# Kernel optimization log

Hardware: AMD Instinct MI355X
Metric: run time of the kernel (lower is better)

The kernel has to match this reference:

```python
import jax, jax.numpy as jnp
import numpy as np

B, L, DL, DM, K = 8192, 1, 1024, 1024, 8


def setup_inputs() -> dict:
    key = jax.random.key(0)
    ks = jax.random.split(key, 8)
    s = lambda k, shape, sc=1.0: jax.random.normal(k, shape, jnp.float32) * sc
    return {
        "l_hidden": s(ks[0], (B, L, DL)),
        "m_hidden": s(ks[1], (B, L, DM)),
        "G_l_m": s(ks[2], (DL, K, DM)),   # randn'd each fwd in torch; exposed as input
        "G_m_l": s(ks[3], (DM, K, DL)),
        "l_fc1_w": s(ks[4], (256, DL), 0.02),
        "l_fc1_b": jnp.zeros((256,), jnp.float32),
        "l_fc2_w": s(ks[5], (DL, 256), 0.02),
        "l_fc2_b": jnp.zeros((DL,), jnp.float32),
        "m_fc1_w": s(ks[6], (128, DM), 0.02),
        "m_fc1_b": jnp.zeros((128,), jnp.float32),
        "m_fc2_w": s(ks[7], (DM, 128), 0.02),
        "m_fc2_b": jnp.zeros((DM,), jnp.float32),
    }


def _cross(h_a, h_b, G, g_vec):
    """One direction of the cross-share unit.
    h_a: [B,L,Da], h_b: [B,L,Db], G: [Da,K,Db], g_vec: [B,L,Da]. L must be 1.
    Broadcasts G over batch instead of torch's .repeat (same math, no 256GB copy).
    """
    b, l, da = h_a.shape
    k = G.shape[1]
    # l_hidden @ reshape(G, [Da, K*Db]) -> reshape to [B, L*K, Db]
    s = jnp.einsum('bld,dke->blke', h_a, G).reshape(b, l * k, -1)      # [B,L*K,Db]
    # tanh( shared @ h_b^T ) -> [B, L*K, L]
    t = jnp.tanh(jnp.einsum('bke,bse->bks', s, h_b))                    # [B,L*K,L]
    # reshape [B,L,K,L] -> permute [B,L,L,K] -> [B,L*L,K]
    t = t.reshape(b, l, k, l).transpose(0, 1, 3, 2).reshape(b, l * l, k)
    g = jnp.tile(g_vec, (1, k, 1))                                      # [B,L*K,Da] (L=1 -> [B,K,Da])
    vec = jnp.matmul(t, g)                                              # [B,L*L,Da]
    attn = jax.nn.softmax(vec, axis=-1)
    out = h_a + attn * h_a
    return out, attn


def reference(l_hidden, m_hidden, G_l_m, G_m_l,
              l_fc1_w, l_fc1_b, l_fc2_w, l_fc2_b,
              m_fc1_w, m_fc1_b, m_fc2_w, m_fc2_b):
    # dropout(0.3) is identity in eval mode
    G_vec_l = (l_hidden @ l_fc1_w.T + l_fc1_b) @ l_fc2_w.T + l_fc2_b   # [B,L,DL]
    G_vec_m = (m_hidden @ m_fc1_w.T + m_fc1_b) @ m_fc2_w.T + m_fc2_b   # [B,L,DM]
    l_out, l_attn = _cross(l_hidden, m_hidden, G_l_m, G_vec_l)
    m_out, m_attn = _cross(m_hidden, l_hidden, G_m_l, G_vec_m)
    return l_out, m_out, l_attn, m_attn
```

## Files before the change

### kernel.cpp

```cpp
#include <hip/hip_runtime.h>


#define NB 8192
#define DD 1024

typedef __bf16 bf16x8 __attribute__((ext_vector_type(8)));
typedef float f32x4 __attribute__((ext_vector_type(4)));

__device__ __forceinline__ unsigned short f2bf(float f) {
  unsigned u = __float_as_uint(f);
  u += 0x7FFFu + ((u >> 16) & 1u);
  return (unsigned short)(u >> 16);
}
__device__ __forceinline__ float bf2f(unsigned short h) {
  return __uint_as_float(((unsigned)h) << 16);
}

__global__ __launch_bounds__(256) void split_cast_k(
    const float* __restrict__ in, unsigned short* __restrict__ hi,
    unsigned short* __restrict__ lo, int n4) {
  int i = blockIdx.x * 256 + threadIdx.x;
  if (i >= n4) return;
  float4 v = reinterpret_cast<const float4*>(in)[i];
  float vv[4] = {v.x, v.y, v.z, v.w};
  unsigned short hh[4], ll[4];
#pragma unroll
  for (int c = 0; c < 4; ++c) {
    hh[c] = f2bf(vv[c]);
    ll[c] = f2bf(vv[c] - bf2f(hh[c]));
  }
  reinterpret_cast<ushort4*>(hi)[i] = make_ushort4(hh[0], hh[1], hh[2], hh[3]);
  reinterpret_cast<ushort4*>(lo)[i] = make_ushort4(ll[0], ll[1], ll[2], ll[3]);
}

__global__ __launch_bounds__(256) void transpose_split_k(
    const float* __restrict__ G, unsigned short* __restrict__ bhi,
    unsigned short* __restrict__ blo) {
  __shared__ float t[32][33];
  int c0 = blockIdx.x * 32;
  int d0 = blockIdx.y * 32;
  int tx = threadIdx.x & 31;
  int tg = threadIdx.x >> 5;
#pragma unroll
  for (int s = 0; s < 4; ++s) {
    int dr = tg * 4 + s;
    t[dr][tx] = G[(size_t)(d0 + dr) * 8192 + c0 + tx];
  }
  __syncthreads();
#pragma unroll
  for (int s = 0; s < 4; ++s) {
    int cr = tg * 4 + s;
    float v = t[tx][cr];
    size_t o = (size_t)(c0 + cr) * 1024 + d0 + tx;
    unsigned short h = f2bf(v);
    bhi[o] = h;
    blo[o] = f2bf(v - bf2f(h));
  }
}

__global__ __launch_bounds__(256) void wct_k(
    const float* __restrict__ w1, const float* __restrict__ b1,
    const float* __restrict__ w2, const float* __restrict__ b2, int J,
    unsigned short* __restrict__ bhi, unsigned short* __restrict__ blo,
    float* __restrict__ bc) {
  __shared__ float w2row[256];
  int n = blockIdx.x;
  int tid = threadIdx.x;
  if (tid < J) w2row[tid] = w2[n * J + tid];
  __syncthreads();
#pragma unroll
  for (int s = 0; s < 4; ++s) {
    int i = tid + s * 256;
    float acc = 0.f;
    for (int j = 0; j < J; ++j) acc = fmaf(w2row[j], w1[j * 1024 + i], acc);
    size_t o = (size_t)(8192 + n) * 1024 + i;
    unsigned short h = f2bf(acc);
    bhi[o] = h;
    blo[o] = f2bf(acc - bf2f(h));
  }
  if (tid == 0) {
    float acc = 0.f;
    for (int j = 0; j < J; ++j) acc = fmaf(w2row[j], b1[j], acc);
    bc[n] = acc + b2[n];
  }
}

#define SBAR() do { asm volatile("" ::: "memory"); __builtin_amdgcn_s_barrier(); asm volatile("" ::: "memory"); } while (0)
#define WAITV0() asm volatile("s_waitcnt vmcnt(0)" ::: "memory")
#define WAITV2() asm volatile("s_waitcnt vmcnt(2)" ::: "memory")

#define GLOAD(SRC, DST)                                              \
  __builtin_amdgcn_global_load_lds(                                  \
      (const __attribute__((address_space(1))) void*)(SRC),          \
      (__attribute__((address_space(3))) void*)(lds + (DST)), 16, 0, 0)

__global__ __launch_bounds__(512, 2) void gemm_k(
    const unsigned short* __restrict__ Ahi_, const unsigned short* __restrict__ Alo_,
    const unsigned short* __restrict__ Bhi_, const unsigned short* __restrict__ Blo_,
    const float* __restrict__ hb, float* __restrict__ gvec, float* __restrict__ x) {
  __shared__ __align__(16) char lds[131072];
  const char* Ah = (const char*)Ahi_;
  const char* Al = (const char*)Alo_;
  const char* Bh = (const char*)Bhi_;
  const char* Bl = (const char*)Blo_;

  const int tid = threadIdx.x;
  const int lane = tid & 63;
  const int wid = tid >> 6;
  const int wm = wid >> 2, wn = wid & 3;

  const int bid = blockIdx.x;
  const int xcd = bid & 7;
  const int j = bid >> 3;
  const int by = xcd * 4 + (j & 3);
  const int bx = j >> 2;
  const int m0 = by * 256;
  const int n0 = bx * 256;
  const bool isg = (n0 >= 8192);
  const int nt = isg ? 16 : 48;

  const int rowl = tid >> 3;
  const int colsw = ((tid & 7) ^ ((tid >> 3) & 7)) << 4;
  const int s0 = ((lane >> 4) ^ (lane & 7)) << 4;
  const int s1 = s0 ^ 64;

  f32x4 acc[4][4][2] = {};

  auto stage = [&](int tl, int q) {
    if (tl >= nt) return;
    const int seg = tl >> 4;
    const char* mat;
    int rowbase, dst;
    if (q < 2) {
      mat = (seg == 1) ? Al : Ah;
      rowbase = m0 + q * 128;
      dst = (tl & 1) * 32768 + q * 16384;
    } else {
      mat = (seg == 2) ? Bl : Bh;
      rowbase = n0 + (q - 2) * 128;
      dst = 65536 + (tl & 1) * 32768 + (q - 2) * 16384;
    }
    const char* src = mat + (size_t)(rowbase + rowl) * 2048 + ((tl & 15) << 7) + colsw;
    dst += wid * 1024;
    GLOAD(src, dst);
    GLOAD(src + 64 * 2048, dst + 8192);
  };

  auto ldA = [&](bf16x8 (*d)[2], int qa, int cb) {
    const char* p = lds + cb + qa * 16384 + (wm * 64 + (lane & 15)) * 128;
#pragma unroll
    for (int f = 0; f < 4; ++f) {
      d[f][0] = *reinterpret_cast<const bf16x8*>(p + f * 2048 + s0);
      d[f][1] = *reinterpret_cast<const bf16x8*>(p + f * 2048 + s1);
    }
  };
  auto ldB = [&](bf16x8 (*d)[2], int qb, int cb) {
    const char* p = lds + 65536 + cb + qb * 16384 + (wn * 32 + (lane & 15)) * 128;
#pragma unroll
    for (int g = 0; g < 2; ++g) {
      d[g][0] = *reinterpret_cast<const bf16x8*>(p + g * 2048 + s0);
      d[g][1] = *reinterpret_cast<const bf16x8*>(p + g * 2048 + s1);
    }
  };
  auto mm = [&](f32x4 (*ac)[2], bf16x8 (*aa)[2], bf16x8 (*bb)[2]) {
#pragma unroll
    for (int f = 0; f < 4; ++f)
#pragma unroll
      for (int g = 0; g < 2; ++g) {
        ac[f][g] = __builtin_amdgcn_mfma_f32_16x16x32_bf16(aa[f][0], bb[g][0], ac[f][g], 0, 0, 0);
        ac[f][g] = __builtin_amdgcn_mfma_f32_16x16x32_bf16(aa[f][1], bb[g][1], ac[f][g], 0, 0, 0);
      }
  };

  stage(0, 0); stage(0, 2); stage(0, 3); stage(0, 1);
  WAITV2();
  SBAR();

  bf16x8 af[4][2], af2[4][2], bv[2][2], bv2[2][2];
  for (int t = 0; t < nt; ++t) {
    const int cb = (t & 1) * 32768;
    ldA(af, 0, cb);
    ldB(bv, 0, cb);
    ldB(bv2, 1, cb);
    stage(t + 1, 0);
    __builtin_amdgcn_s_setprio(1);
    mm(acc[0], af, bv);
    __builtin_amdgcn_s_setprio(0);
    if (t + 1 < nt) { WAITV2(); } else { WAITV0(); }
    SBAR();
    ldA(af2, 1, cb);
    stage(t + 1, 2);
    __builtin_amdgcn_s_setprio(1);
    mm(acc[1], af, bv2);
    __builtin_amdgcn_s_setprio(0);
    SBAR();
    stage(t + 1, 3);
    __builtin_amdgcn_s_setprio(1);
    mm(acc[2], af2, bv2);
    __builtin_amdgcn_s_setprio(0);
    SBAR();
    stage(t + 1, 1);
    __builtin_amdgcn_s_setprio(1);
    mm(acc[3], af2, bv);
    __builtin_amdgcn_s_setprio(0);
    WAITV2();
    SBAR();
  }

  const int coll = lane & 15;
  const int rg = (lane >> 4) * 4;
  if (isg) {
#pragma unroll
    for (int q = 0; q < 4; ++q) {
      const int qm = (q >= 2);
      const int qn = (q == 1 || q == 2);
#pragma unroll
      for (int f = 0; f < 4; ++f)
#pragma unroll
        for (int rr = 0; rr < 4; ++rr) {
          const int row = m0 + qm * 128 + wm * 64 + f * 16 + rg + rr;
#pragma unroll
          for (int g = 0; g < 2; ++g) {
            const int gcol = (n0 - 8192) + qn * 128 + wn * 32 + g * 16 + coll;
            gvec[(size_t)row * 1024 + gcol] = acc[q][f][g][rr];
          }
        }
    }
  } else {
    const int kidx = n0 >> 10;
    const int ebase = (n0 & 1023) + wn * 32 + coll;
#pragma unroll
    for (int qm = 0; qm < 2; ++qm) {
      f32x4 (*acA)[2] = acc[qm ? 3 : 0];
      f32x4 (*acB)[2] = acc[qm ? 2 : 1];
#pragma unroll
      for (int f = 0; f < 4; ++f)
#pragma unroll
        for (int rr = 0; rr < 4; ++rr) {
          const int row = m0 + qm * 128 + wm * 64 + f * 16 + rg + rr;
          const float* hr = hb + (size_t)row * 1024 + ebase;
          float tmp = acA[f][0][rr] * hr[0] + acA[f][1][rr] * hr[16] +
                      acB[f][0][rr] * hr[128] + acB[f][1][rr] * hr[144];
#pragma unroll
          for (int s = 1; s < 16; s <<= 1) tmp += __shfl_xor(tmp, s);
          if (coll == 0) atomicAdd(&x[row * 8 + kidx], tmp);
        }
    }
  }
}

__global__ __launch_bounds__(256) void finalize_k(
    const float* __restrict__ xk, const float* __restrict__ gvec,
    const float* __restrict__ bc, const float* __restrict__ ha,
    float* __restrict__ out, float* __restrict__ attn) {
  int b = blockIdx.x;
  int tid = threadIdx.x;
  float S = 0.f;
#pragma unroll
  for (int k = 0; k < 8; ++k) S += tanhf(xk[b * 8 + k]);
  float v[4];
  float mx = -3.4e38f;
#pragma unroll
  for (int s = 0; s < 4; ++s) {
    int d = tid + s * 256;
    v[s] = S * (gvec[(size_t)b * 1024 + d] + bc[d]);
    mx = fmaxf(mx, v[s]);
  }
  __shared__ float red[8];
#pragma unroll
  for (int off = 32; off >= 1; off >>= 1) mx = fmaxf(mx, __shfl_xor(mx, off));
  int lane = tid & 63, w = tid >> 6;
  if (lane == 0) red[w] = mx;
  __syncthreads();
  float m = fmaxf(fmaxf(red[0], red[1]), fmaxf(red[2], red[3]));
  float e[4], sum = 0.f;
#pragma unroll
  for (int s = 0; s < 4; ++s) { e[s] = __expf(v[s] - m); sum += e[s]; }
#pragma unroll
  for (int off = 32; off >= 1; off >>= 1) sum += __shfl_xor(sum, off);
  if (lane == 0) red[4 + w] = sum;
  __syncthreads();
  float inv = 1.f / (red[4] + red[5] + red[6] + red[7]);
#pragma unroll
  for (int s = 0; s < 4; ++s) {
    int d = tid + s * 256;
    float a = e[s] * inv;
    attn[(size_t)b * 1024 + d] = a;
    float h = ha[(size_t)b * 1024 + d];
    out[(size_t)b * 1024 + d] = fmaf(a, h, h);
  }
}

extern "C" void kernel_launch(void* const* d_in, const int* in_sizes, int n_in,
                              void* d_out, int out_size, void* d_ws, size_t ws_size,
                              hipStream_t stream) {
  const float* l_hidden = (const float*)d_in[0];
  const float* m_hidden = (const float*)d_in[1];
  const float* G_l_m = (const float*)d_in[2];
  const float* G_m_l = (const float*)d_in[3];
  const float* l_fc1_w = (const float*)d_in[4];
  const float* l_fc1_b = (const float*)d_in[5];
  const float* l_fc2_w = (const float*)d_in[6];
  const float* l_fc2_b = (const float*)d_in[7];
  const float* m_fc1_w = (const float*)d_in[8];
  const float* m_fc1_b = (const float*)d_in[9];
  const float* m_fc2_w = (const float*)d_in[10];
  const float* m_fc2_b = (const float*)d_in[11];
  float* out = (float*)d_out;

  char* ws = (char*)d_ws;
  unsigned short* Ahi = (unsigned short*)(ws);
  unsigned short* Alo = (unsigned short*)(ws + 16777216);
  unsigned short* Bhi = (unsigned short*)(ws + 33554432);
  unsigned short* Blo = (unsigned short*)(ws + 52428800);
  float* gvec = (float*)(ws + 71303168);
  float* x = (float*)(ws + 104857600);
  float* bc = (float*)(ws + 105381888);

  hipMemsetAsync(x, 0, 2 * NB * 8 * sizeof(float), stream);

  const size_t BD = (size_t)NB * DD;
  dim3 gemmGrid(1152);

  split_cast_k<<<(int)(BD / 4 / 256), 256, 0, stream>>>(l_hidden, Ahi, Alo, (int)(BD / 4));
  transpose_split_k<<<dim3(256, 32), 256, 0, stream>>>(G_l_m, Bhi, Blo);
  wct_k<<<1024, 256, 0, stream>>>(l_fc1_w, l_fc1_b, l_fc2_w, l_fc2_b, 256, Bhi, Blo, bc);
  gemm_k<<<gemmGrid, 512, 0, stream>>>(Ahi, Alo, Bhi, Blo, m_hidden, gvec, x);
  finalize_k<<<NB, 256, 0, stream>>>(x, gvec, bc, l_hidden, out, out + 2 * BD);

  split_cast_k<<<(int)(BD / 4 / 256), 256, 0, stream>>>(m_hidden, Ahi, Alo, (int)(BD / 4));
  transpose_split_k<<<dim3(256, 32), 256, 0, stream>>>(G_m_l, Bhi, Blo);
  wct_k<<<1024, 256, 0, stream>>>(m_fc1_w, m_fc1_b, m_fc2_w, m_fc2_b, 128, Bhi, Blo, bc);
  gemm_k<<<gemmGrid, 512, 0, stream>>>(Ahi, Alo, Bhi, Blo, l_hidden, gvec, x + NB * 8);
  finalize_k<<<NB, 256, 0, stream>>>(x + NB * 8, gvec, bc, m_hidden, out + BD, out + 3 * BD);
}
```

Baseline: 1.060 ms.

## Restructure GEMM main loop into deeper LDS prefetch pipeline with one block per CU

Reworks the 256x256 bf16 MFMA GEMM main loop so LDS fragment reads for the next quadrant and next k-tile are issued ahead of the MFMAs, with explicit lgkmcnt waits and sched barriers. Global-to-LDS staging now runs up to two tiles ahead (vmcnt(4)), and the quadrant order and epilogue accumulator mapping are permuted to match. Launch bounds drop from two blocks per CU to one, freeing registers for the extra fragment buffers at the cost of occupancy. The clamped tail tiles reissue redundant loads instead of skipping them.

```diff
diff --git a/kernel.cpp b/kernel.cpp
--- a/kernel.cpp
+++ b/kernel.cpp
@@ -86,15 +86,16 @@
 }
 
 #define SBAR() do { asm volatile("" ::: "memory"); __builtin_amdgcn_s_barrier(); asm volatile("" ::: "memory"); } while (0)
-#define WAITV0() asm volatile("s_waitcnt vmcnt(0)" ::: "memory")
+#define LGK0() do { asm volatile("s_waitcnt lgkmcnt(0)" ::: "memory"); __builtin_amdgcn_sched_barrier(0); } while (0)
 #define WAITV2() asm volatile("s_waitcnt vmcnt(2)" ::: "memory")
+#define WAITV4() asm volatile("s_waitcnt vmcnt(4)" ::: "memory")
 
 #define GLOAD(SRC, DST)                                              \
   __builtin_amdgcn_global_load_lds(                                  \
       (const __attribute__((address_space(1))) void*)(SRC),          \
       (__attribute__((address_space(3))) void*)(lds + (DST)), 16, 0, 0)
 
-__global__ __launch_bounds__(512, 2) void gemm_k(
+__global__ __launch_bounds__(512, 1) void gemm_k(
     const unsigned short* __restrict__ Ahi_, const unsigned short* __restrict__ Alo_,
     const unsigned short* __restrict__ Bhi_, const unsigned short* __restrict__ Blo_,
     const float* __restrict__ hb, float* __restrict__ gvec, float* __restrict__ x) {
@@ -126,19 +127,18 @@
 
   f32x4 acc[4][4][2] = {};
 
-  auto stage = [&](int tl, int q) {
-    if (tl >= nt) return;
+  auto stage = [&](int tl, int par, int q) {
     const int seg = tl >> 4;
     const char* mat;
     int rowbase, dst;
     if (q < 2) {
       mat = (seg == 1) ? Al : Ah;
       rowbase = m0 + q * 128;
-      dst = (tl & 1) * 32768 + q * 16384;
+      dst = par * 32768 + q * 16384;
     } else {
       mat = (seg == 2) ? Bl : Bh;
       rowbase = n0 + (q - 2) * 128;
-      dst = 65536 + (tl & 1) * 32768 + (q - 2) * 16384;
+      dst = 65536 + par * 32768 + (q - 2) * 16384;
     }
     const char* src = mat + (size_t)(rowbase + rowl) * 2048 + ((tl & 15) << 7) + colsw;
     dst += wid * 1024;
@@ -172,38 +172,57 @@
       }
   };
 
-  stage(0, 0); stage(0, 2); stage(0, 3); stage(0, 1);
+  bf16x8 af[4][2], af2[4][2], bv[2][2], bv2[2][2];
+
+  stage(0, 0, 0); stage(0, 0, 2); stage(0, 0, 1); stage(0, 0, 3);
   WAITV2();
   SBAR();
-
-  bf16x8 af[4][2], af2[4][2], bv[2][2], bv2[2][2];
+  ldA(af, 0, 0);
+  ldB(bv, 0, 0);
+  stage(1, 1, 2);
+
   for (int t = 0; t < nt; ++t) {
     const int cb = (t & 1) * 32768;
-    ldA(af, 0, cb);
-    ldB(bv, 0, cb);
-    ldB(bv2, 1, cb);
-    stage(t + 1, 0);
+    const int cbN = cb ^ 32768;
+    const int parN = (t + 1) & 1;
+    const int parN2 = t & 1;
+    const int tn = (t + 1 < nt) ? (t + 1) : (nt - 1);
+    const int tn2 = (t + 2 < nt) ? (t + 2) : (nt - 1);
+    ldA(af2, 1, cb);
+    stage(tn, parN, 0);
+    SBAR();
+    LGK0();
     __builtin_amdgcn_s_setprio(1);
     mm(acc[0], af, bv);
     __builtin_amdgcn_s_setprio(0);
-    if (t + 1 < nt) { WAITV2(); } else { WAITV0(); }
-    SBAR();
-    ldA(af2, 1, cb);
-    stage(t + 1, 2);
+    WAITV4();
+    SBAR();
+    ldB(bv2, 1, cb);
+    stage(tn, parN, 1);
+    SBAR();
+    LGK0();
     __builtin_amdgcn_s_setprio(1);
-    mm(acc[1], af, bv2);
+    mm(acc[1], af2, bv);
     __builtin_amdgcn_s_setprio(0);
-    SBAR();
-    stage(t + 1, 3);
+    WAITV4();
+    SBAR();
+    ldB(bv, 0, cbN);
+    stage(tn, parN, 3);
+    SBAR();
+    LGK0();
     __builtin_amdgcn_s_setprio(1);
-    mm(acc[2], af2, bv2);
+    mm(acc[2], af, bv2);
     __builtin_amdgcn_s_setprio(0);
-    SBAR();
-    stage(t + 1, 1);
+    WAITV4();
+    SBAR();
+    ldA(af, 0, cbN);
+    stage(tn2, parN2, 2);
+    SBAR();
+    LGK0();
     __builtin_amdgcn_s_setprio(1);
-    mm(acc[3], af2, bv);
+    mm(acc[3], af2, bv2);
     __builtin_amdgcn_s_setprio(0);
-    WAITV2();
+    WAITV4();
     SBAR();
   }
 
@@ -212,8 +231,8 @@
   if (isg) {
 #pragma unroll
     for (int q = 0; q < 4; ++q) {
-      const int qm = (q >= 2);
-      const int qn = (q == 1 || q == 2);
+      const int qm = q & 1;
+      const int qn = q >> 1;
 #pragma unroll
       for (int f = 0; f < 4; ++f)
 #pragma unroll
@@ -231,8 +250,8 @@
     const int ebase = (n0 & 1023) + wn * 32 + coll;
 #pragma unroll
     for (int qm = 0; qm < 2; ++qm) {
-      f32x4 (*acA)[2] = acc[qm ? 3 : 0];
-      f32x4 (*acB)[2] = acc[qm ? 2 : 1];
+      f32x4 (*acA)[2] = acc[qm ? 1 : 0];
+      f32x4 (*acB)[2] = acc[qm ? 3 : 2];
 #pragma unroll
       for (int f = 0; f < 4; ++f)
 #pragma unroll
```

Result: slower. 1.084 ms (+2.2%).

## Restructure GEMM main loop prefetch schedule and use single-block occupancy

Applied to the files above, without the earlier changes.

Reorders the K-loop so the next tile's A/B quadrants are staged in pairs and the first fragments of the next tile are read from LDS before the loop iteration ends. This cuts the loop from four barriers to two per iteration and replaces partial vmcnt waits with full waits. The launch bound drops from 2 to 1 blocks per SM, allowing more registers for the extra prefetched fragments. The trade-off is lower occupancy and coarser waits, which can expose memory latency. On the last iteration it issues redundant loads of the final tile instead of skipping them.

```diff
diff --git a/kernel.cpp b/kernel.cpp
--- a/kernel.cpp
+++ b/kernel.cpp
@@ -87,14 +87,13 @@
 
 #define SBAR() do { asm volatile("" ::: "memory"); __builtin_amdgcn_s_barrier(); asm volatile("" ::: "memory"); } while (0)
 #define WAITV0() asm volatile("s_waitcnt vmcnt(0)" ::: "memory")
-#define WAITV2() asm volatile("s_waitcnt vmcnt(2)" ::: "memory")
 
 #define GLOAD(SRC, DST)                                              \
   __builtin_amdgcn_global_load_lds(                                  \
       (const __attribute__((address_space(1))) void*)(SRC),          \
       (__attribute__((address_space(3))) void*)(lds + (DST)), 16, 0, 0)
 
-__global__ __launch_bounds__(512, 2) void gemm_k(
+__global__ __launch_bounds__(512, 1) void gemm_k(
     const unsigned short* __restrict__ Ahi_, const unsigned short* __restrict__ Alo_,
     const unsigned short* __restrict__ Bhi_, const unsigned short* __restrict__ Blo_,
     const float* __restrict__ hb, float* __restrict__ gvec, float* __restrict__ x) {
@@ -126,19 +125,18 @@
 
   f32x4 acc[4][4][2] = {};
 
-  auto stage = [&](int tl, int q) {
-    if (tl >= nt) return;
+  auto stage = [&](int tl, int par, int q) {
     const int seg = tl >> 4;
     const char* mat;
     int rowbase, dst;
     if (q < 2) {
       mat = (seg == 1) ? Al : Ah;
       rowbase = m0 + q * 128;
-      dst = (tl & 1) * 32768 + q * 16384;
+      dst = par * 32768 + q * 16384;
     } else {
       mat = (seg == 2) ? Bl : Bh;
       rowbase = n0 + (q - 2) * 128;
-      dst = 65536 + (tl & 1) * 32768 + (q - 2) * 16384;
+      dst = 65536 + par * 32768 + (q - 2) * 16384;
     }
     const char* src = mat + (size_t)(rowbase + rowl) * 2048 + ((tl & 15) << 7) + colsw;
     dst += wid * 1024;
@@ -172,38 +170,43 @@
       }
   };
 
-  stage(0, 0); stage(0, 2); stage(0, 3); stage(0, 1);
-  WAITV2();
+  bf16x8 af[4][2], af2[4][2], bv[2][2], bv2[2][2];
+
+  stage(0, 0, 0); stage(0, 0, 2); stage(0, 0, 1); stage(0, 0, 3);
+  WAITV0();
   SBAR();
-
-  bf16x8 af[4][2], af2[4][2], bv[2][2], bv2[2][2];
+  ldA(af, 0, 0);
+  ldB(bv, 0, 0);
+
   for (int t = 0; t < nt; ++t) {
     const int cb = (t & 1) * 32768;
-    ldA(af, 0, cb);
-    ldB(bv, 0, cb);
+    const int cbN = cb ^ 32768;
+    const int parN = (t + 1) & 1;
+    const int tn = (t + 1 < nt) ? (t + 1) : (nt - 1);
     ldB(bv2, 1, cb);
-    stage(t + 1, 0);
+    stage(tn, parN, 0);
+    stage(tn, parN, 2);
     __builtin_amdgcn_s_setprio(1);
     mm(acc[0], af, bv);
     __builtin_amdgcn_s_setprio(0);
-    if (t + 1 < nt) { WAITV2(); } else { WAITV0(); }
-    SBAR();
     ldA(af2, 1, cb);
-    stage(t + 1, 2);
     __builtin_amdgcn_s_setprio(1);
     mm(acc[1], af, bv2);
     __builtin_amdgcn_s_setprio(0);
+    WAITV0();
     SBAR();
-    stage(t + 1, 3);
+    ldA(af, 0, cbN);
+    stage(tn, parN, 1);
+    stage(tn, parN, 3);
     __builtin_amdgcn_s_setprio(1);
     mm(acc[2], af2, bv2);
     __builtin_amdgcn_s_setprio(0);
-    SBAR();
-    stage(t + 1, 1);
     __builtin_amdgcn_s_setprio(1);
     mm(acc[3], af2, bv);
     __builtin_amdgcn_s_setprio(0);
-    WAITV2();
+    __builtin_amdgcn_sched_barrier(0);
+    ldB(bv, 0, cbN);
+    WAITV0();
     SBAR();
   }
 
```

Measured after the change: 1.054 ms. No clear change (-0.6%).
